# Kernel optimization log

Measured on AMD Instinct MI355X. Metric: run time of the kernel, lower is better.

## Reference

```python
import jax, jax.numpy as jnp
import numpy as np

HIDDEN = 512
HEADS = 8
HEAD_DIM = HIDDEN // HEADS
INNER = int(HIDDEN * 4.0)
MAX_DIST = 512
LN_EPS = 1e-5


def _layernorm(x, g, b):
    mu = jnp.mean(x, axis=-1, keepdims=True)
    var = jnp.var(x, axis=-1, keepdims=True)
    return (x - mu) * jax.lax.rsqrt(var + LN_EPS) * g + b


def setup_inputs() -> dict:
    key = jax.random.key(0)
    ks = jax.random.split(key, 12)
    B, T = 4, 2048
    s = 0.02
    return {
        "x": jax.random.normal(ks[0], (B, T, HIDDEN), dtype=jnp.float32),
        "w_qkv": jax.random.normal(ks[1], (HIDDEN, 3 * HIDDEN), dtype=jnp.float32) * s,
        "b_qkv": jnp.zeros((3 * HIDDEN,), dtype=jnp.float32),
        "w_out": jax.random.normal(ks[2], (HIDDEN, HIDDEN), dtype=jnp.float32) * s,
        "b_out": jnp.zeros((HIDDEN,), dtype=jnp.float32),
        "ln1_g": jnp.ones((HIDDEN,), dtype=jnp.float32),
        "ln1_b": jnp.zeros((HIDDEN,), dtype=jnp.float32),
        "ln2_g": jnp.ones((HIDDEN,), dtype=jnp.float32),
        "ln2_b": jnp.zeros((HIDDEN,), dtype=jnp.float32),
        "w_mlp1": jax.random.normal(ks[3], (HIDDEN, INNER), dtype=jnp.float32) * s,
        "b_mlp1": jnp.zeros((INNER,), dtype=jnp.float32),
        "w_mlp2": jax.random.normal(ks[4], (INNER, HIDDEN), dtype=jnp.float32) * s,
        "b_mlp2": jnp.zeros((HIDDEN,), dtype=jnp.float32),
        "rel_table": jax.random.normal(ks[5], (2 * MAX_DIST + 1, HEADS), dtype=jnp.float32) * s,
    }


def reference(x, w_qkv, b_qkv, w_out, b_out, ln1_g, ln1_b, ln2_g, ln2_b,
              w_mlp1, b_mlp1, w_mlp2, b_mlp2, rel_table):
    B, T, C = x.shape
    scale = HEAD_DIM ** -0.5
    qkv = x @ w_qkv + b_qkv  # [B,T,3C]
    qkv = qkv.reshape(B, T, 3, HEADS, HEAD_DIM)
    q = qkv[:, :, 0].transpose(0, 2, 1, 3)  # [B,H,T,D]
    k = qkv[:, :, 1].transpose(0, 2, 1, 3)
    v = qkv[:, :, 2].transpose(0, 2, 1, 3)
    logits = jnp.einsum('bhqd,bhkd->bhqk', q, k) * scale
    # relative position bias: clamp(q_pos - k_pos) lookup -> [H,T,T]
    rel = jnp.clip(jnp.arange(T)[:, None] - jnp.arange(T)[None, :], -MAX_DIST, MAX_DIST) + MAX_DIST
    bias = rel_table[rel].transpose(2, 0, 1)  # [H,T,T]
    logits = logits + bias[None]
    attn = jax.nn.softmax(logits, axis=-1)
    out = jnp.einsum('bhqk,bhkd->bhqd', attn, v)
    out = out.transpose(0, 2, 1, 3).reshape(B, T, C)
    out = out @ w_out + b_out
    x = _layernorm(x + out, ln1_g, ln1_b)
    h = jax.nn.gelu(x @ w_mlp1 + b_mlp1, approximate=False)
    mlp_out = h @ w_mlp2 + b_mlp2
    return _layernorm(x + mlp_out, ln2_g, ln2_b)
```

## Files before the change

kernel.cpp:

```cpp
#include <hip/hip_runtime.h>
#include <hip/hip_bf16.h>

using bf16 = __hip_bfloat16;
typedef __attribute__((ext_vector_type(8))) short bf16x8;
typedef __attribute__((ext_vector_type(4))) short bf16x4;
typedef __attribute__((ext_vector_type(4))) float f32x4;

#define HIDDEN 512
#define HEADS 8
#define HDIM 64
#define INNER 2048
#define MAXD 512
#define BB 4
#define TT 2048
#define MM (BB*TT)
#define LOG2E 1.44269504088896340736f

typedef const __attribute__((address_space(1))) unsigned int* gas_u32p;
typedef __attribute__((address_space(3))) unsigned int* las_u32p;

__device__ __forceinline__ void gload_lds16(const void* g, void* l) {
    __builtin_amdgcn_global_load_lds((gas_u32p)g, (las_u32p)l, 16, 0, 0);
}
__device__ __forceinline__ short bfr(float x) {
    return (short)__bfloat16_as_ushort(__float2bfloat16(x));
}
__device__ __forceinline__ float bf2f(short u) {
    return __uint_as_float(((unsigned)(unsigned short)u) << 16);
}

__global__ __launch_bounds__(256) void prep_kernel(
    const float* __restrict__ x, const float* __restrict__ w_qkv,
    const float* __restrict__ w_out, const float* __restrict__ w1,
    const float* __restrict__ w2,
    bf16* __restrict__ xb, bf16* __restrict__ wqkv_t, bf16* __restrict__ wout_t,
    bf16* __restrict__ w1_t, bf16* __restrict__ w2_t)
{
    __shared__ float tile[32][33];
    int bid = blockIdx.x;
    if (bid < 4096) {
        int i = (bid * 256 + threadIdx.x) * 4;
        float4 v = *(const float4*)&x[i];
        bf16 o[4] = {__float2bfloat16(v.x), __float2bfloat16(v.y),
                     __float2bfloat16(v.z), __float2bfloat16(v.w)};
        *(bf16x4*)&xb[i] = *(bf16x4*)o;
        return;
    }
    bid -= 4096;
    const float* in; bf16* out; int K, N, bx, by;
    if (bid < 768)       { in = w_qkv; out = wqkv_t; K = 512;  N = 1536; bx = bid % 48; by = bid / 48; }
    else if (bid < 1024) { bid -= 768;  in = w_out; out = wout_t; K = 512;  N = 512;  bx = bid % 16; by = bid / 16; }
    else if (bid < 2048) { bid -= 1024; in = w1;   out = w1_t;   K = 512;  N = 2048; bx = bid % 64; by = bid / 64; }
    else                 { bid -= 2048; in = w2;   out = w2_t;   K = 2048; N = 512;  bx = bid % 16; by = bid / 16; }
    int lx = threadIdx.x & 31, ly = threadIdx.x >> 5;
    #pragma unroll
    for (int i = 0; i < 4; ++i)
        tile[ly + 8*i][lx] = in[(size_t)(by*32 + ly + 8*i) * N + bx*32 + lx];
    __syncthreads();
    #pragma unroll
    for (int i = 0; i < 4; ++i)
        out[(size_t)(bx*32 + ly + 8*i) * K + by*32 + lx] =
            __float2bfloat16(tile[lx][ly + 8*i]);
}

template<int EPI, int BN, int VT, int RESID>
__global__ __launch_bounds__(256) void gemm_kernel(
    const bf16* __restrict__ A, const bf16* __restrict__ BT,
    const float* __restrict__ bias, const void* __restrict__ resid,
    bf16* __restrict__ C, bf16* __restrict__ vt_out,
    int M, int N, int K)
{
    constexpr int NBF = BN / 32;
    constexpr int NBS = BN / 64;
    constexpr int BBYTES = BN * 64;
    __shared__ __align__(16) bf16 As[2][128*32];
    __shared__ __align__(16) bf16 Bs[2][BN*32];
    const int tid = threadIdx.x;
    const int wid = tid >> 6;
    const int lane = tid & 63;
    const int lhi = lane >> 4, llo = lane & 15;
    const int m0 = blockIdx.x * 128, n0 = blockIdx.y * BN;
    const int wr = wid >> 1, wc = wid & 1;

    const int srow = tid >> 2;
    const int scol = ((tid & 3) ^ ((srow >> 1) & 3)) * 8;
    const bf16* Ap = A + (size_t)(m0 + srow) * K + scol;
    const bf16* Bp = BT + (size_t)(n0 + srow) * K + scol;
    const size_t step64 = (size_t)64 * K;
    const int rsw = (llo >> 1) & 3;

    f32x4 acc[4][NBF] = {};

    auto STAGE = [&](int k1, int bi) {
        #pragma unroll
        for (int rr = 0; rr < 2; ++rr)
            gload_lds16(Ap + k1 + rr*step64, (char*)As + bi*8192 + rr*4096 + tid*16);
        #pragma unroll
        for (int rr = 0; rr < NBS; ++rr)
            gload_lds16(Bp + k1 + rr*step64, (char*)Bs + bi*BBYTES + rr*4096 + tid*16);
    };

    STAGE(0, 0);

    const int NK = K >> 5;
    for (int it = 0; it < NK; ++it) {
        const int p = it & 1;
        __syncthreads();
        if (it + 1 < NK) STAGE((it + 1) << 5, p^1);
        bf16x8 af[4], bfrg[NBF];
        #pragma unroll
        for (int ar = 0; ar < 4; ++ar)
            af[ar] = *(const bf16x8*)((const char*)As + p*8192 +
                       (64*wr + 16*ar + llo)*64 + ((lhi ^ rsw) << 4));
        #pragma unroll
        for (int bc = 0; bc < NBF; ++bc)
            bfrg[bc] = *(const bf16x8*)((const char*)Bs + p*BBYTES +
                       ((BN/2)*wc + 16*bc + llo)*64 + ((lhi ^ rsw) << 4));
        #pragma unroll
        for (int ar = 0; ar < 4; ++ar)
            #pragma unroll
            for (int bc = 0; bc < NBF; ++bc)
                acc[ar][bc] = __builtin_amdgcn_mfma_f32_16x16x32_bf16(
                    af[ar], bfrg[bc], acc[ar][bc], 0, 0, 0);
    }

    if (VT && n0 >= 1024) {
        #pragma unroll
        for (int ar = 0; ar < 4; ++ar) {
            const int row = m0 + 64*wr + 16*ar + 4*lhi;
            const int bq = row >> 11, t0 = row & 2047;
            #pragma unroll
            for (int bc = 0; bc < NBF; ++bc) {
                const int cv = n0 - 1024 + (BN/2)*wc + 16*bc + llo;
                const int h = cv >> 6, d = cv & 63;
                float bv = bias[n0 + (BN/2)*wc + 16*bc + llo];
                bf16x4 pk = {bfr(acc[ar][bc][0] + bv), bfr(acc[ar][bc][1] + bv),
                             bfr(acc[ar][bc][2] + bv), bfr(acc[ar][bc][3] + bv)};
                *(bf16x4*)&vt_out[(((size_t)(bq*8 + h) * 64 + d) << 11) + t0] = pk;
            }
        }
        return;
    }

    #pragma unroll
    for (int ar = 0; ar < 4; ++ar) {
        #pragma unroll
        for (int j = 0; j < 4; ++j) {
            int row = m0 + 64*wr + 16*ar + 4*lhi + j;
            #pragma unroll
            for (int bc = 0; bc < NBF; ++bc) {
                int col = n0 + (BN/2)*wc + 16*bc + llo;
                float v = acc[ar][bc][j] + bias[col];
                if (RESID == 1)
                    v += ((const float*)resid)[(size_t)row * N + col];
                if (RESID == 2)
                    v += __bfloat162float(((const bf16*)resid)[(size_t)row * N + col]);
                if (EPI == 2) {
                    float u = 0.7978845608028654f * (v + 0.044715f * v * v * v);
                    float e = __builtin_amdgcn_exp2f(u * (2.0f * LOG2E));
                    v = v * (1.0f - 1.0f / (1.0f + e));
                }
                C[(size_t)row * N + col] = __float2bfloat16(v);
            }
        }
    }
}

#define PTN (TT + 128)
__global__ __launch_bounds__(512) void attn_kernel(
    const bf16* __restrict__ qkv,
    const bf16* __restrict__ v_t,
    const float* __restrict__ rel_table,
    bf16* __restrict__ attn_out)
{
    __shared__ __align__(16) char smem[49152 + PTN*4];
    char* KsB = smem;
    char* VsB = smem + 16384;
    char* PsB = smem + 32768;
    float* PT = (float*)(smem + 49152);

    const int qt = blockIdx.x, bh = blockIdx.y;
    const int b = bh >> 3, h = bh & 7;
    const int tid = threadIdx.x, wid = tid >> 6, lane = tid & 63;
    const int lhi = lane >> 4, llo = lane & 15;
    const int gw = wid >> 2;
    const int wq = wid & 3;

    const int lo = qt*128 - (TT - 1);
    for (int i = tid; i < PTN; i += 512) {
        int idx = min(max(i + lo, -MAXD), MAXD) + MAXD;
        PT[i] = rel_table[(size_t)idx * HEADS + h] * LOG2E;
    }

    const int qb = qt * 128;
    const int q0w = qb + wq * 32;
    bf16x8 bq[2][2];
    #pragma unroll
    for (int qh = 0; qh < 2; ++qh)
        #pragma unroll
        for (int kc = 0; kc < 2; ++kc)
            bq[qh][kc] = *(const bf16x8*)&qkv[(size_t)(b*TT + q0w + qh*16 + llo) * 1536
                                              + h*64 + kc*32 + lhi*8];

    bf16x8 aones;
    #pragma unroll
    for (int i = 0; i < 8; ++i) aones[i] = (short)0x3F80;

    const int so = tid * 16;
    const int kg = so >> 12;
    const int kr = (so >> 7) & 31;
    const int kc0 = (((so & 127) ^ ((kr & 7) << 4)) >> 1);
    const int vd = (so >> 7) & 63;
    const int vbs = (so & 127) ^ ((vd & 7) << 4);
    const int vg = vbs >> 6;
    const int vke = (vbs & 63) >> 1;

    const bf16* kbase = qkv + (size_t)(b*TT) * 1536 + 512 + h*64;
    const bf16* vbase = v_t + (size_t)bh * 64 * TT;

    f32x4 accLf[2] = {};
    f32x4 accO[2][4] = {};

    gload_lds16(kbase + (size_t)(kg*32 + kr) * 1536 + kc0, KsB + so);
    gload_lds16(vbase + (size_t)vd * TT + vg*32 + vke,     VsB + so);
    __syncthreads();

    const float cFut  = PT[min(max(-512 - lo, 0), PTN - 1)];
    const float cPast = PT[min(max( 512 - lo, 0), PTN - 1)];
    const float sc = 0.125f * LOG2E;
    const int ibq = wq*32 + llo + (TT - 1) - 4*lhi;

    for (int it = 0; it < 32; ++it) {
        const int p = it & 1;
        const int kv0 = it*64 + gw*32;
        if (it) __syncthreads();
        if (it + 1 < 32) {
            const int kn = (it + 1) * 64;
            gload_lds16(kbase + (size_t)(kn + kg*32 + kr) * 1536 + kc0, KsB + (p^1)*8192 + so);
            gload_lds16(vbase + (size_t)vd * TT + kn + vg*32 + vke,     VsB + (p^1)*8192 + so);
        }
        const char* Kb = KsB + p*8192 + gw*4096;
        const char* Vb = VsB + p*8192;

        f32x4 s[2][2] = {};
        __builtin_amdgcn_s_setprio(1);
        #pragma unroll
        for (int f = 0; f < 2; ++f) {
            const int rr = 16*f + llo;
            #pragma unroll
            for (int kc = 0; kc < 2; ++kc) {
                bf16x8 ak = *(const bf16x8*)(Kb + rr*128 + (((4*kc + lhi) ^ (rr & 7)) << 4));
                #pragma unroll
                for (int qh = 0; qh < 2; ++qh)
                    s[qh][f] = __builtin_amdgcn_mfma_f32_16x16x32_bf16(
                        ak, bq[qh][kc], s[qh][f], 0, 0, 0);
            }
        }
        __builtin_amdgcn_s_setprio(0);

        if (kv0 >= qb + 639) {
            #pragma unroll
            for (int qh = 0; qh < 2; ++qh)
                #pragma unroll
                for (int f = 0; f < 2; ++f)
                    #pragma unroll
                    for (int j = 0; j < 4; ++j)
                        s[qh][f][j] = fmaf(s[qh][f][j], sc, cFut);
        } else if (kv0 <= qb - 543) {
            #pragma unroll
            for (int qh = 0; qh < 2; ++qh)
                #pragma unroll
                for (int f = 0; f < 2; ++f)
                    #pragma unroll
                    for (int j = 0; j < 4; ++j)
                        s[qh][f][j] = fmaf(s[qh][f][j], sc, cPast);
        } else {
            const int ib = ibq - kv0;
            #pragma unroll
            for (int qh = 0; qh < 2; ++qh)
                #pragma unroll
                for (int f = 0; f < 2; ++f)
                    #pragma unroll
                    for (int j = 0; j < 4; ++j)
                        s[qh][f][j] = fmaf(s[qh][f][j], sc, PT[ib + qh*16 - 16*f - j]);
        }

        #pragma unroll
        for (int qh = 0; qh < 2; ++qh) {
            #pragma unroll
            for (int f = 0; f < 2; ++f) {
                float p0 = __builtin_amdgcn_exp2f(s[qh][f][0]);
                float p1 = __builtin_amdgcn_exp2f(s[qh][f][1]);
                float p2 = __builtin_amdgcn_exp2f(s[qh][f][2]);
                float p3 = __builtin_amdgcn_exp2f(s[qh][f][3]);
                bf16x4 pk = {bfr(p0), bfr(p1), bfr(p2), bfr(p3)};
                *(bf16x4*)(PsB + wid*2048 + llo*128 +
                           ((qh*64 + f*32 + lhi*8) ^ ((llo & 7) << 4))) = pk;
            }
        }

        bf16x8 pf[2];
        #pragma unroll
        for (int qh = 0; qh < 2; ++qh)
            pf[qh] = *(const bf16x8*)(PsB + wid*2048 + llo*128 +
                                      ((qh*64 + lhi*16) ^ ((llo & 7) << 4)));
        __builtin_amdgcn_s_setprio(1);
        #pragma unroll
        for (int fd = 0; fd < 4; ++fd) {
            const int rv = 16*fd + llo;
            bf16x8 av = *(const bf16x8*)(Vb + rv*128 +
                         ((gw*64 + lhi*16) ^ ((rv & 7) << 4)));
            #pragma unroll
            for (int qh = 0; qh < 2; ++qh)
                accO[qh][fd] = __builtin_amdgcn_mfma_f32_16x16x32_bf16(
                    av, pf[qh], accO[qh][fd], 0, 0, 0);
        }
        #pragma unroll
        for (int qh = 0; qh < 2; ++qh)
            accLf[qh] = __builtin_amdgcn_mfma_f32_16x16x32_bf16(
                aones, pf[qh], accLf[qh], 0, 0, 0);
        __builtin_amdgcn_s_setprio(0);
    }

    __syncthreads();
    float* xbuf = (float*)smem;
    if (gw == 1) {
        float* dst = xbuf + (size_t)(wq*64 + lane) * 34;
        #pragma unroll
        for (int qh = 0; qh < 2; ++qh)
            #pragma unroll
            for (int fd = 0; fd < 4; ++fd)
                #pragma unroll
                for (int j = 0; j < 4; ++j)
                    dst[qh*16 + fd*4 + j] = accO[qh][fd][j];
        dst[32] = accLf[0][0]; dst[33] = accLf[1][0];
    }
    __syncthreads();
    if (gw == 0) {
        const float* src = xbuf + (size_t)(wq*64 + lane) * 34;
        #pragma unroll
        for (int qh = 0; qh < 2; ++qh) {
            const float rl = 1.0f / (accLf[qh][0] + src[32 + qh]);
            const int row = b*TT + q0w + qh*16 + llo;
            #pragma unroll
            for (int fd = 0; fd < 4; ++fd) {
                bf16x4 ov = {bfr((accO[qh][fd][0] + src[qh*16 + fd*4 + 0]) * rl),
                             bfr((accO[qh][fd][1] + src[qh*16 + fd*4 + 1]) * rl),
                             bfr((accO[qh][fd][2] + src[qh*16 + fd*4 + 2]) * rl),
                             bfr((accO[qh][fd][3] + src[qh*16 + fd*4 + 3]) * rl)};
                *(bf16x4*)&attn_out[(size_t)row * HIDDEN + h*64 + 16*fd + 4*lhi] = ov;
            }
        }
    }
}

template<int WB>
__global__ __launch_bounds__(256) void ln_kernel(
    const bf16* __restrict__ in,
    const float* __restrict__ g, const float* __restrict__ bb,
    float* __restrict__ of, bf16* __restrict__ ob)
{
    int row = blockIdx.x * 4 + (threadIdx.x >> 6);
    int lane = threadIdx.x & 63;
    const bf16* pa = in + (size_t)row * HIDDEN + lane * 8;
    bf16x8 v8 = *(const bf16x8*)pa;
    float v[8];
    float s = 0.f, sq = 0.f;
    #pragma unroll
    for (int j = 0; j < 8; ++j) {
        v[j] = bf2f(v8[j]);
        s += v[j]; sq += v[j] * v[j];
    }
    #pragma unroll
    for (int d = 1; d < 64; d <<= 1) {
        s  += __shfl_xor(s,  d, 64);
        sq += __shfl_xor(sq, d, 64);
    }
    float mean = s * (1.f / HIDDEN);
    float var  = sq * (1.f / HIDDEN) - mean * mean;
    float rstd = rsqrtf(var + 1e-5f);
    float o[8];
    #pragma unroll
    for (int j = 0; j < 8; ++j) {
        int col = lane * 8 + j;
        o[j] = (v[j] - mean) * rstd * g[col] + bb[col];
    }
    if (WB) {
        bf16x8 ov;
        #pragma unroll
        for (int j = 0; j < 8; ++j) ov[j] = bfr(o[j]);
        *(bf16x8*)&ob[(size_t)row * HIDDEN + lane * 8] = ov;
    } else {
        float4 o0 = {o[0], o[1], o[2], o[3]};
        float4 o1 = {o[4], o[5], o[6], o[7]};
        *(float4*)&of[(size_t)row * HIDDEN + lane * 8]     = o0;
        *(float4*)&of[(size_t)row * HIDDEN + lane * 8 + 4] = o1;
    }
}

extern "C" void kernel_launch(void* const* d_in, const int* in_sizes, int n_in,
                              void* d_out, int out_size, void* d_ws, size_t ws_size,
                              hipStream_t stream) {
    const float* x     = (const float*)d_in[0];
    const float* w_qkv = (const float*)d_in[1];
    const float* b_qkv = (const float*)d_in[2];
    const float* w_out = (const float*)d_in[3];
    const float* b_out = (const float*)d_in[4];
    const float* ln1_g = (const float*)d_in[5];
    const float* ln1_b = (const float*)d_in[6];
    const float* ln2_g = (const float*)d_in[7];
    const float* ln2_b = (const float*)d_in[8];
    const float* w1    = (const float*)d_in[9];
    const float* b1    = (const float*)d_in[10];
    const float* w2    = (const float*)d_in[11];
    const float* b2    = (const float*)d_in[12];
    const float* rel   = (const float*)d_in[13];
    float* out = (float*)d_out;

    char* ws = (char*)d_ws;
    bf16*  xb     = (bf16*)(ws + 0);
    bf16*  wqkv_t = (bf16*)(ws + 8388608);
    bf16*  wout_t = (bf16*)(ws + 9961472);
    bf16*  w1_t   = (bf16*)(ws + 10485760);
    bf16*  w2_t   = (bf16*)(ws + 12582912);
    bf16*  qkv    = (bf16*)(ws + 14680064);
    bf16*  v_t    = (bf16*)(ws + 39845888);
    bf16*  attn_o = (bf16*)(ws + 48234496);
    bf16*  proj   = (bf16*)(ws + 56623104);
    bf16*  h      = (bf16*)(ws + 14680064);
    bf16*  x1b    = (bf16*)(ws + 90177536);

    prep_kernel<<<7168, 256, 0, stream>>>(x, w_qkv, w_out, w1, w2,
                                          xb, wqkv_t, wout_t, w1_t, w2_t);
    gemm_kernel<0,128,1,0><<<dim3(MM/128, 1536/128), 256, 0, stream>>>(
        xb, wqkv_t, b_qkv, nullptr, qkv, v_t, MM, 1536, 512);
    attn_kernel<<<dim3(TT/128, BB*HEADS), 512, 0, stream>>>(qkv, v_t, rel, attn_o);
    gemm_kernel<0,64,0,1><<<dim3(MM/128, 512/64), 256, 0, stream>>>(
        attn_o, wout_t, b_out, x, proj, nullptr, MM, 512, 512);
    ln_kernel<1><<<MM/4, 256, 0, stream>>>(proj, ln1_g, ln1_b, nullptr, x1b);
    gemm_kernel<2,128,0,0><<<dim3(MM/128, 2048/128), 256, 0, stream>>>(
        x1b, w1_t, b1, nullptr, h, nullptr, MM, 2048, 512);
    gemm_kernel<0,64,0,2><<<dim3(MM/128, 512/64), 256, 0, stream>>>(
        h, w2_t, b2, x1b, proj, nullptr, MM, 512, 2048);
    ln_kernel<0><<<MM/4, 256, 0, stream>>>(proj, ln2_g, ln2_b, out, nullptr);
}
```

Baseline: 176.4 us.

## Split-K the second MLP GEMM and sum partials inside final layernorm

The K=2048 MLP down-projection GEMM is split into two K halves along a new grid z dimension. This doubles the block count from 512 to 1024 to fill the GPU better. Each half writes its own bf16 partial, and only the second half adds the bias. A new layernorm kernel then adds the residual and both partials before normalizing. The cost is extra global traffic for the second partial buffer, plus extra rounding because the partials are stored in bf16.

Result: no change. 175.3 us, median of 2 (-0.6%).

```diff
diff --git a/kernel.cpp b/kernel.cpp
--- a/kernel.cpp
+++ b/kernel.cpp
@@ -63,7 +63,7 @@
             __float2bfloat16(tile[lx][ly + 8*i]);
 }
 
-template<int EPI, int BN, int VT, int RESID>
+template<int EPI, int BN, int VT, int RESID, int SPLITK>
 __global__ __launch_bounds__(256) void gemm_kernel(
     const bf16* __restrict__ A, const bf16* __restrict__ BT,
     const float* __restrict__ bias, const void* __restrict__ resid,
@@ -82,6 +82,15 @@
     const int m0 = blockIdx.x * 128, n0 = blockIdx.y * BN;
     const int wr = wid >> 1, wc = wid & 1;
 
+    int kz = 0, KL = K;
+    if (SPLITK) {
+        kz = blockIdx.z;
+        KL = K >> 1;
+        A  += (size_t)kz * KL;
+        BT += (size_t)kz * KL;
+        C  += (size_t)kz * M * N;
+    }
+
     const int srow = tid >> 2;
     const int scol = ((tid & 3) ^ ((srow >> 1) & 3)) * 8;
     const bf16* Ap = A + (size_t)(m0 + srow) * K + scol;
@@ -102,7 +111,7 @@
 
     STAGE(0, 0);
 
-    const int NK = K >> 5;
+    const int NK = KL >> 5;
     for (int it = 0; it < NK; ++it) {
         const int p = it & 1;
         __syncthreads();
@@ -150,7 +159,8 @@
             #pragma unroll
             for (int bc = 0; bc < NBF; ++bc) {
                 int col = n0 + (BN/2)*wc + 16*bc + llo;
-                float v = acc[ar][bc][j] + bias[col];
+                float v = acc[ar][bc][j];
+                if (!SPLITK || kz == 1) v += bias[col];
                 if (RESID == 1)
                     v += ((const float*)resid)[(size_t)row * N + col];
                 if (RESID == 2)
@@ -396,6 +406,45 @@
         *(float4*)&of[(size_t)row * HIDDEN + lane * 8]     = o0;
         *(float4*)&of[(size_t)row * HIDDEN + lane * 8 + 4] = o1;
     }
+}
+
+__global__ __launch_bounds__(256) void ln3_kernel(
+    const bf16* __restrict__ in0, const bf16* __restrict__ in1,
+    const bf16* __restrict__ in2,
+    const float* __restrict__ g, const float* __restrict__ bb,
+    float* __restrict__ of)
+{
+    int row = blockIdx.x * 4 + (threadIdx.x >> 6);
+    int lane = threadIdx.x & 63;
+    const size_t off = (size_t)row * HIDDEN + lane * 8;
+    bf16x8 a8 = *(const bf16x8*)&in0[off];
+    bf16x8 b8 = *(const bf16x8*)&in1[off];
+    bf16x8 c8 = *(const bf16x8*)&in2[off];
+    float v[8];
+    float s = 0.f, sq = 0.f;
+    #pragma unroll
+    for (int j = 0; j < 8; ++j) {
+        v[j] = bf2f(a8[j]) + bf2f(b8[j]) + bf2f(c8[j]);
+        s += v[j]; sq += v[j] * v[j];
+    }
+    #pragma unroll
+    for (int d = 1; d < 64; d <<= 1) {
+        s  += __shfl_xor(s,  d, 64);
+        sq += __shfl_xor(sq, d, 64);
+    }
+    float mean = s * (1.f / HIDDEN);
+    float var  = sq * (1.f / HIDDEN) - mean * mean;
+    float rstd = rsqrtf(var + 1e-5f);
+    float o[8];
+    #pragma unroll
+    for (int j = 0; j < 8; ++j) {
+        int col = lane * 8 + j;
+        o[j] = (v[j] - mean) * rstd * g[col] + bb[col];
+    }
+    float4 o0 = {o[0], o[1], o[2], o[3]};
+    float4 o1 = {o[4], o[5], o[6], o[7]};
+    *(float4*)&of[off]     = o0;
+    *(float4*)&of[off + 4] = o1;
 }
 
 extern "C" void kernel_launch(void* const* d_in, const int* in_sizes, int n_in,
@@ -432,15 +481,16 @@
 
     prep_kernel<<<7168, 256, 0, stream>>>(x, w_qkv, w_out, w1, w2,
                                           xb, wqkv_t, wout_t, w1_t, w2_t);
-    gemm_kernel<0,128,1,0><<<dim3(MM/128, 1536/128), 256, 0, stream>>>(
+    gemm_kernel<0,128,1,0,0><<<dim3(MM/128, 1536/128), 256, 0, stream>>>(
         xb, wqkv_t, b_qkv, nullptr, qkv, v_t, MM, 1536, 512);
     attn_kernel<<<dim3(TT/128, BB*HEADS), 512, 0, stream>>>(qkv, v_t, rel, attn_o);
-    gemm_kernel<0,64,0,1><<<dim3(MM/128, 512/64), 256, 0, stream>>>(
+    gemm_kernel<0,64,0,1,0><<<dim3(MM/128, 512/64), 256, 0, stream>>>(
         attn_o, wout_t, b_out, x, proj, nullptr, MM, 512, 512);
     ln_kernel<1><<<MM/4, 256, 0, stream>>>(proj, ln1_g, ln1_b, nullptr, x1b);
-    gemm_kernel<2,128,0,0><<<dim3(MM/128, 2048/128), 256, 0, stream>>>(
+    gemm_kernel<2,128,0,0,0><<<dim3(MM/128, 2048/128), 256, 0, stream>>>(
         x1b, w1_t, b1, nullptr, h, nullptr, MM, 2048, 512);
-    gemm_kernel<0,64,0,2><<<dim3(MM/128, 512/64), 256, 0, stream>>>(
-        h, w2_t, b2, x1b, proj, nullptr, MM, 512, 2048);
-    ln_kernel<0><<<MM/4, 256, 0, stream>>>(proj, ln2_g, ln2_b, out, nullptr);
-}
+    gemm_kernel<0,64,0,0,1><<<dim3(MM/128, 512/64, 2), 256, 0, stream>>>(
+        h, w2_t, b2, nullptr, proj, nullptr, MM, 512, 2048);
+    ln3_kernel<<<MM/4, 256, 0, stream>>>(x1b, proj, proj + (size_t)MM*512,
+                                         ln2_g, ln2_b, out);
+}
```
